# Performance work log

Hardware: AMD Instinct MI355X
Metric: run time of the kernel (lower is better)

Reference implementation:

```python
import jax, jax.numpy as jnp
import numpy as np

D_MODEL = 4096
NUM_HEADS = 64
DEPTH = D_MODEL // NUM_HEADS  # 64
B = 64   # must equal NUM_HEADS (quirk of original rope-after-split-heads code)
S = 64   # must equal NUM_HEADS (S*DEPTH must equal D_MODEL)


def setup_inputs() -> dict:
    key = jax.random.key(0)
    ks = jax.random.split(key, 9)
    scale = 1.0 / np.sqrt(D_MODEL)
    d = {"x": jax.random.normal(ks[0], (B, S, D_MODEL), dtype=jnp.float32)}
    for i, n in enumerate(["q", "k", "v", "o"]):
        d[f"w_{n}"] = jax.random.normal(ks[1 + i], (D_MODEL, D_MODEL), dtype=jnp.float32) * scale
        d[f"b_{n}"] = jax.random.normal(ks[5 + i], (D_MODEL,), dtype=jnp.float32) * 0.01
    return d


def _rope(x):
    # Faithful to the original: rope is applied to (B, H, S, depth) and treats
    # dim 1 (heads) as the 'sequence' axis, with inv_freq sized for full d_model.
    inv_freq = 1.0 / (10000.0 ** (jnp.arange(0, D_MODEL, 2, dtype=jnp.float32) / D_MODEL))
    pos = jnp.arange(x.shape[1], dtype=jnp.float32)[:, None]       # (H, 1)
    sinusoid = pos * inv_freq                                       # (H, d_model/2)
    sin = jnp.sin(sinusoid)[None, :, None, :]                       # (1, H, 1, d_model/2)
    cos = jnp.cos(sinusoid)[None, :, None, :]
    xr = x.reshape(x.shape[0], x.shape[1], -1, 2)                   # (B, H, S*depth/2, 2)
    real, imag = xr[..., 0], xr[..., 1]                             # (B, H, M) with M == d_model/2
    rot_real = real * cos - imag * sin                              # broadcasts to (1, B, H, M)
    rot_imag = real * sin + imag * cos
    return jnp.stack((rot_real, rot_imag), axis=-1).reshape(x.shape)


def reference(x, w_q, b_q, w_k, b_k, w_v, b_v, w_o, b_o):
    def split_heads(t):  # (B, S, d_model) -> (B, H, S, depth)
        return t.reshape(B, S, NUM_HEADS, DEPTH).transpose(0, 2, 1, 3)

    q = split_heads(x @ w_q.T + b_q)
    k = split_heads(x @ w_k.T + b_k)
    v = split_heads(x @ w_v.T + b_v)
    q = _rope(q)
    k = _rope(k)

    scores = jnp.einsum("bhqd,bhkd->bhqk", q, k) / np.sqrt(DEPTH).astype(np.float32)
    weights = jax.nn.softmax(scores, axis=-1)
    out = jnp.einsum("bhqk,bhkd->bhqd", weights, v)
    out = out.transpose(0, 2, 1, 3).reshape(B, S, D_MODEL)
    return out @ w_o.T + b_o
```

## Files before the change

kernel.cpp:

```cpp
#include <hip/hip_runtime.h>
#include <cstdint>
#include <cstddef>


typedef _Float16 half8 __attribute__((ext_vector_type(8)));
typedef float floatx4 __attribute__((ext_vector_type(4)));

#define NELT_W 16777216u
#define NEG_LOG2_10000_OVER_2048 (-0.0064881408103278559f)

__device__ __forceinline__ void gl_lds16(const void* g, void* l) {
    __builtin_amdgcn_global_load_lds(
        (const __attribute__((address_space(1))) void*)(void*)g,
        (__attribute__((address_space(3))) void*)l,
        16, 0, 0);
}

__global__ __launch_bounds__(256) void cast5_kernel(
    const float* __restrict__ x,  const float* __restrict__ wq,
    const float* __restrict__ wk, const float* __restrict__ wv,
    const float* __restrict__ wo,
    _Float16* __restrict__ xh, _Float16* __restrict__ wcat,
    _Float16* __restrict__ woh)
{
    const float* s;
    _Float16* d;
    switch (blockIdx.y) {
        case 0:  s = x;  d = xh;                 break;
        case 1:  s = wq; d = wcat;               break;
        case 2:  s = wk; d = wcat + NELT_W;      break;
        case 3:  s = wv; d = wcat + 2 * NELT_W;  break;
        default: s = wo; d = woh;                break;
    }
    int i0 = (blockIdx.x * 256 + threadIdx.x) * 8;
    int stride = gridDim.x * 256 * 8;
    for (int i = i0; i < (int)NELT_W; i += stride) {
        const float4 a = *(const float4*)(s + i);
        const float4 b = *(const float4*)(s + i + 4);
        half8 h;
        h[0] = (_Float16)a.x; h[1] = (_Float16)a.y;
        h[2] = (_Float16)a.z; h[3] = (_Float16)a.w;
        h[4] = (_Float16)b.x; h[5] = (_Float16)b.y;
        h[6] = (_Float16)b.z; h[7] = (_Float16)b.w;
        *(half8*)(d + i) = h;
    }
}

__global__ __launch_bounds__(256) void biascat_kernel(
    const float* __restrict__ bq, const float* __restrict__ bk,
    const float* __restrict__ bv, float* __restrict__ out)
{
    int i = blockIdx.x * 256 + threadIdx.x;
    if (i < 4096) {
        out[i]        = bq[i];
        out[4096 + i] = bk[i];
        out[8192 + i] = bv[i];
    }
}


#define STAGE(gb_, lb_, kt_, half_) do {                                      \
    const int R0_ = (half_) << 7;                                             \
    gl_lds16((gb_) + (size_t)R0_ * K + (kt_), (lb_) + R0_ * 64);              \
    gl_lds16((gb_) + (size_t)(R0_ + 64) * K + (kt_), (lb_) + (R0_ + 64) * 64);\
} while (0)

#define LDA2(bo_, ha_, m0_) do {                                              \
    const _Float16* pa_ = As + (bo_) + (size_t)(((ha_) << 7) + wg2 + fr) * 64;\
    _Pragma("unroll") for (int mt_ = (m0_); mt_ < (m0_) + 2; ++mt_) {         \
        af[mt_][0] = *(const half8*)(pa_ + mt_ * 1024 + sw0);                 \
        af[mt_][1] = *(const half8*)(pa_ + mt_ * 1024 + sw1);                 \
    }                                                                         \
} while (0)

#define LDB4(bo_, hb_, dst_) do {                                             \
    const _Float16* pb_ = Bs + (bo_) + (size_t)(((hb_) << 7) + wn2 + fr) * 64;\
    _Pragma("unroll") for (int nt_ = 0; nt_ < 2; ++nt_) {                     \
        dst_[nt_][0] = *(const half8*)(pb_ + nt_ * 1024 + sw0);               \
        dst_[nt_][1] = *(const half8*)(pb_ + nt_ * 1024 + sw1);               \
    }                                                                         \
} while (0)

#define MFMAQ(qm_, qn_, bq_) do {                                             \
    _Pragma("unroll") for (int s_ = 0; s_ < 2; ++s_)                          \
    _Pragma("unroll") for (int mt_ = 0; mt_ < 4; ++mt_)                       \
    _Pragma("unroll") for (int nt_ = 0; nt_ < 2; ++nt_)                       \
        acc[(qm_) * 4 + mt_][(qn_) * 2 + nt_] =                               \
            __builtin_amdgcn_mfma_f32_16x16x32_f16(                           \
                af[mt_][s_], bq_[nt_][s_],                                    \
                acc[(qm_) * 4 + mt_][(qn_) * 2 + nt_], 0, 0, 0);              \
} while (0)

#define TILE() do {                                                           \
    const int kt1_ = (t + 1) << 6;                                            \
    const int kt2_ = (t + 2) << 6;                                            \
    const bool s1_ = (t + 1 < NT);                                            \
    const bool s2_ = (t + 2 < NT);                                            \
                       \
    LDB4(bufo, 1, bq1);                                                       \
    if (s1_) STAGE(Ab, AsT + nbufo, kt1_, 1);                                 \
    __builtin_amdgcn_s_barrier();                                             \
    __builtin_amdgcn_s_setprio(1);                                            \
    MFMAQ(0, 0, bq0);                                                         \
    __builtin_amdgcn_s_setprio(0);                                            \
    __builtin_amdgcn_s_barrier();                                             \
             \
    if (s2_) STAGE(Ab, AsT + bufo, kt2_, 0);                                  \
    __builtin_amdgcn_s_barrier();                                             \
    __builtin_amdgcn_s_setprio(1);                                            \
    MFMAQ(0, 1, bq1);                                                         \
    __builtin_amdgcn_s_setprio(0);                                            \
    LDA2(bufo, 1, 0);                        \
    __builtin_amdgcn_s_barrier();                                             \
       \
    LDA2(bufo, 1, 2);                                                         \
    if (s2_) STAGE(Bb, BsT + bufo, kt2_, 0);                                  \
    __builtin_amdgcn_s_barrier();                                             \
    __builtin_amdgcn_s_setprio(1);                                            \
    MFMAQ(1, 0, bq0);                                                         \
    __builtin_amdgcn_s_setprio(0);                                            \
    __builtin_amdgcn_s_barrier();                                             \
        \
    if (s2_) STAGE(Bb, BsT + bufo, kt2_, 1);                                  \
    if (t < NT - 2) asm volatile("s_waitcnt vmcnt(6)" ::: "memory");          \
    else            asm volatile("s_waitcnt vmcnt(0)" ::: "memory");          \
    __builtin_amdgcn_s_barrier();                                             \
    __builtin_amdgcn_sched_barrier(0);   \
    if (s1_) LDB4(nbufo, 0, bq0);         \
    __builtin_amdgcn_s_setprio(1);                                            \
    MFMAQ(1, 1, bq1);                                                         \
    __builtin_amdgcn_s_setprio(0);                                            \
    if (s1_) { LDA2(nbufo, 0, 0); LDA2(nbufo, 0, 2); }          \
    __builtin_amdgcn_s_barrier();                                             \
} while (0)

template <int OUT_F16>
__global__ __launch_bounds__(512, 2) void gemm_nt_256(
    const _Float16* __restrict__ A, const _Float16* __restrict__ B,
    const float* __restrict__ bias, void* __restrict__ Cout,
    int M, int N, int K)
{
    __shared__ __align__(16) _Float16 As[2 * 256 * 64];
    __shared__ __align__(16) _Float16 Bs[2 * 256 * 64];

    const int tid = threadIdx.x;
    const int nwg  = gridDim.x;
    const int swz  = (blockIdx.x & 7) * (nwg >> 3) + (blockIdx.x >> 3);
    const int gn   = N >> 8;
    const int row0 = (swz / gn) << 8;
    const int col0 = (swz % gn) << 8;

    const int wave = tid >> 6;
    const int lane = tid & 63;
    const int wg2 = (wave >> 2) << 6;
    const int wn2 = (wave & 3) << 5;

    const int fr  = lane & 15;
    const int g4  = lane >> 4;
    const int sw0 = ((g4 ^ (fr & 7)) << 3);
    const int sw1 = (((4 + g4) ^ (fr & 7)) << 3);

    const int srow = tid >> 3;
    const int scol = ((tid & 7) ^ (srow & 7)) << 3;
    const _Float16* Ab = A + (size_t)(row0 + srow) * K + scol;
    const _Float16* Bb = B + (size_t)(col0 + srow) * K + scol;
    _Float16* AsT = As + tid * 8;
    _Float16* BsT = Bs + tid * 8;

    floatx4 acc[8][4];
#pragma unroll
    for (int i = 0; i < 8; i++)
#pragma unroll
        for (int j = 0; j < 4; j++) acc[i][j] = (floatx4){0.f, 0.f, 0.f, 0.f};

    half8 af[4][2], bq0[2][2], bq1[2][2];

    const int NT = K >> 6;

    STAGE(Ab, AsT, 0, 0);
    STAGE(Ab, AsT, 0, 1);
    STAGE(Bb, BsT, 0, 0);
    STAGE(Bb, BsT, 0, 1);
    STAGE(Ab, AsT + 16384, 64, 0);
    STAGE(Bb, BsT + 16384, 64, 0);
    STAGE(Bb, BsT + 16384, 64, 1);
    asm volatile("s_waitcnt vmcnt(6)" ::: "memory");
    __builtin_amdgcn_s_barrier();
    __builtin_amdgcn_sched_barrier(0);
    LDB4(0, 0, bq0);
    LDA2(0, 0, 0);
    LDA2(0, 0, 2);

    for (int tt = 0; tt < NT; tt += 2) {
        { const int t = tt;     const int bufo = 0;     const int nbufo = 16384; TILE(); }
        { const int t = tt + 1; const int bufo = 16384; const int nbufo = 0;     TILE(); }
    }

    const int crow = row0 + wg2 + (g4 << 2);
    const int ccol = col0 + wn2 + fr;
#pragma unroll
    for (int mi = 0; mi < 8; mi++) {
#pragma unroll
        for (int ni = 0; ni < 4; ni++) {
            const int gc = ccol + ((ni >> 1) << 7) + ((ni & 1) << 4);
            const float bv = bias[gc];
#pragma unroll
            for (int r2 = 0; r2 < 4; r2++) {
                const int gr = crow + ((mi >> 2) << 7) + ((mi & 3) << 4) + r2;
                const float v = acc[mi][ni][r2] + bv;
                if (OUT_F16)
                    ((_Float16*)Cout)[(size_t)gr * N + gc] = (_Float16)v;
                else
                    ((float*)Cout)[(size_t)gr * N + gc] = v;
            }
        }
    }
    (void)M;
}

__global__ __launch_bounds__(256) void attn_kernel(
    const _Float16* __restrict__ qkv, _Float16* __restrict__ out)
{
    __shared__ __align__(16) _Float16 qs[64][72];
    __shared__ __align__(16) _Float16 ks[64][72];
    __shared__ __align__(16) _Float16 vt[64][72];
    __shared__ __align__(16) _Float16 ps[4][16][72];

    const int tid  = threadIdx.x;
    const int bb   = blockIdx.x >> 6;
    const int hh   = blockIdx.x & 63;
    const int wave = tid >> 6;
    const int lane = tid & 63;
    const int r  = tid >> 2;
    const int cb = (tid & 3) * 8;
    const float fb = (float)bb;

    const _Float16* grow = qkv + (size_t)(bb * 64 + r) * 12288 + hh * 64;

#pragma unroll
    for (int u = 0; u < 2; u++) {
        const int c8 = cb + u * 32;
        half8 q8 = *(const half8*)(grow + c8);
        half8 k8 = *(const half8*)(grow + 4096 + c8);
        half8 v8 = *(const half8*)(grow + 8192 + c8);
#pragma unroll
        for (int p = 0; p < 4; p++) {
            const int m = r * 32 + (c8 >> 1) + p;
            const float theta = fb * exp2f((float)m * NEG_LOG2_10000_OVER_2048);
            float sn, cs;
            __sincosf(theta, &sn, &cs);
            const float qe = (float)q8[2 * p], qo = (float)q8[2 * p + 1];
            q8[2 * p]     = (_Float16)(qe * cs - qo * sn);
            q8[2 * p + 1] = (_Float16)(qe * sn + qo * cs);
            const float ke = (float)k8[2 * p], ko = (float)k8[2 * p + 1];
            k8[2 * p]     = (_Float16)(ke * cs - ko * sn);
            k8[2 * p + 1] = (_Float16)(ke * sn + ko * cs);
        }
        *(half8*)&qs[r][c8] = q8;
        *(half8*)&ks[r][c8] = k8;
#pragma unroll
        for (int j = 0; j < 8; j++) vt[c8 + j][r] = v8[j];
    }
    __syncthreads();

    const int fr = lane & 15;
    const int fc = (lane >> 4) * 8;

    floatx4 sa[4];
#pragma unroll
    for (int t = 0; t < 4; t++) sa[t] = (floatx4){0.f, 0.f, 0.f, 0.f};
    half8 a0 = *(const half8*)&qs[wave * 16 + fr][fc];
    half8 a1 = *(const half8*)&qs[wave * 16 + fr][fc + 32];
#pragma unroll
    for (int t = 0; t < 4; t++) {
        half8 kb0 = *(const half8*)&ks[t * 16 + fr][fc];
        half8 kb1 = *(const half8*)&ks[t * 16 + fr][fc + 32];
        sa[t] = __builtin_amdgcn_mfma_f32_16x16x32_f16(a0, kb0, sa[t], 0, 0, 0);
        sa[t] = __builtin_amdgcn_mfma_f32_16x16x32_f16(a1, kb1, sa[t], 0, 0, 0);
    }

#pragma unroll
    for (int i = 0; i < 4; i++) {
        float mx = -1e30f;
#pragma unroll
        for (int t = 0; t < 4; t++) mx = fmaxf(mx, sa[t][i]);
#pragma unroll
        for (int d = 1; d < 16; d <<= 1) mx = fmaxf(mx, __shfl_xor(mx, d));
        float sum = 0.f;
        float pv[4];
#pragma unroll
        for (int t = 0; t < 4; t++) {
            const float e = __expf((sa[t][i] - mx) * 0.125f);
            pv[t] = e;
            sum += e;
        }
#pragma unroll
        for (int d = 1; d < 16; d <<= 1) sum += __shfl_xor(sum, d);
        const float inv = 1.0f / sum;
        const int prow = ((lane >> 4) << 2) + i;
#pragma unroll
        for (int t = 0; t < 4; t++)
            ps[wave][prow][t * 16 + fr] = (_Float16)(pv[t] * inv);
    }

    half8 pa0 = *(const half8*)&ps[wave][fr][fc];
    half8 pa1 = *(const half8*)&ps[wave][fr][fc + 32];
    floatx4 oa[4];
#pragma unroll
    for (int t = 0; t < 4; t++) oa[t] = (floatx4){0.f, 0.f, 0.f, 0.f};
#pragma unroll
    for (int t = 0; t < 4; t++) {
        half8 vb0 = *(const half8*)&vt[t * 16 + fr][fc];
        half8 vb1 = *(const half8*)&vt[t * 16 + fr][fc + 32];
        oa[t] = __builtin_amdgcn_mfma_f32_16x16x32_f16(pa0, vb0, oa[t], 0, 0, 0);
        oa[t] = __builtin_amdgcn_mfma_f32_16x16x32_f16(pa1, vb1, oa[t], 0, 0, 0);
    }

    _Float16* obase = out + (size_t)(bb * 64) * 4096 + hh * 64;
#pragma unroll
    for (int t = 0; t < 4; t++)
#pragma unroll
        for (int i = 0; i < 4; i++) {
            const int sq = wave * 16 + ((lane >> 4) << 2) + i;
            obase[(size_t)sq * 4096 + t * 16 + fr] = (_Float16)oa[t][i];
        }
}

extern "C" void kernel_launch(void* const* d_in, const int* in_sizes, int n_in,
                              void* d_out, int out_size, void* d_ws, size_t ws_size,
                              hipStream_t stream)
{
    const float* x  = (const float*)d_in[0];
    const float* wq = (const float*)d_in[1];
    const float* bq = (const float*)d_in[2];
    const float* wk = (const float*)d_in[3];
    const float* bk = (const float*)d_in[4];
    const float* wv = (const float*)d_in[5];
    const float* bv = (const float*)d_in[6];
    const float* wo = (const float*)d_in[7];
    const float* bo = (const float*)d_in[8];

    char* ws = (char*)d_ws;
    _Float16* xh      = (_Float16*)(ws);
    _Float16* wcat    = (_Float16*)(ws + 33554432);
    _Float16* woh     = (_Float16*)(ws + 134217728);
    _Float16* qkv     = (_Float16*)(ws + 167772160);
    _Float16* attnbuf = (_Float16*)(ws + 268435456);
    float*    biascat = (float*)(ws + 301989888);

    cast5_kernel<<<dim3(1024, 5), dim3(256), 0, stream>>>(
        x, wq, wk, wv, wo, xh, wcat, woh);
    biascat_kernel<<<dim3(16), dim3(256), 0, stream>>>(bq, bk, bv, biascat);

    gemm_nt_256<1><<<dim3(768), dim3(512), 0, stream>>>(
        xh, wcat, biascat, qkv, 4096, 12288, 4096);

    attn_kernel<<<dim3(4096), dim3(256), 0, stream>>>(qkv, attnbuf);

    gemm_nt_256<0><<<dim3(256), dim3(512), 0, stream>>>(
        attnbuf, woh, bo, d_out, 4096, 4096, 4096);
}
```

Measured before the change: 878.3 us.

## Switch GEMM inner loop to 32x32x16 MFMA with restructured LDS fragment loads

```diff
diff --git a/kernel.cpp b/kernel.cpp
--- a/kernel.cpp
+++ b/kernel.cpp
@@ -5,6 +5,7 @@
 
 typedef _Float16 half8 __attribute__((ext_vector_type(8)));
 typedef float floatx4 __attribute__((ext_vector_type(4)));
+typedef float floatx16 __attribute__((ext_vector_type(16)));
 
 #define NELT_W 16777216u
 #define NEG_LOG2_10000_OVER_2048 (-0.0064881408103278559f)
@@ -59,36 +60,37 @@
 }
 
 
+#define BAR()   __builtin_amdgcn_s_barrier()
+#define SB0()   __builtin_amdgcn_sched_barrier(0)
+#define SETP1() __builtin_amdgcn_s_setprio(1)
+#define SETP0() __builtin_amdgcn_s_setprio(0)
+
 #define STAGE(gb_, lb_, kt_, half_) do {                                      \
     const int R0_ = (half_) << 7;                                             \
     gl_lds16((gb_) + (size_t)R0_ * K + (kt_), (lb_) + R0_ * 64);              \
     gl_lds16((gb_) + (size_t)(R0_ + 64) * K + (kt_), (lb_) + (R0_ + 64) * 64);\
 } while (0)
 
-#define LDA2(bo_, ha_, m0_) do {                                              \
-    const _Float16* pa_ = As + (bo_) + (size_t)(((ha_) << 7) + wg2 + fr) * 64;\
-    _Pragma("unroll") for (int mt_ = (m0_); mt_ < (m0_) + 2; ++mt_) {         \
-        af[mt_][0] = *(const half8*)(pa_ + mt_ * 1024 + sw0);                 \
-        af[mt_][1] = *(const half8*)(pa_ + mt_ * 1024 + sw1);                 \
-    }                                                                         \
-} while (0)
-
-#define LDB4(bo_, hb_, dst_) do {                                             \
-    const _Float16* pb_ = Bs + (bo_) + (size_t)(((hb_) << 7) + wn2 + fr) * 64;\
-    _Pragma("unroll") for (int nt_ = 0; nt_ < 2; ++nt_) {                     \
-        dst_[nt_][0] = *(const half8*)(pb_ + nt_ * 1024 + sw0);               \
-        dst_[nt_][1] = *(const half8*)(pb_ + nt_ * 1024 + sw1);               \
-    }                                                                         \
-} while (0)
-
-#define MFMAQ(qm_, qn_, bq_) do {                                             \
-    _Pragma("unroll") for (int s_ = 0; s_ < 2; ++s_)                          \
-    _Pragma("unroll") for (int mt_ = 0; mt_ < 4; ++mt_)                       \
-    _Pragma("unroll") for (int nt_ = 0; nt_ < 2; ++nt_)                       \
-        acc[(qm_) * 4 + mt_][(qn_) * 2 + nt_] =                               \
-            __builtin_amdgcn_mfma_f32_16x16x32_f16(                           \
-                af[mt_][s_], bq_[nt_][s_],                                    \
-                acc[(qm_) * 4 + mt_][(qn_) * 2 + nt_], 0, 0, 0);              \
+#define LDA32(bo_, ha_) do {                                                  \
+    const _Float16* pa_ = As + (bo_) +                                        \
+        (size_t)((((ha_) << 7) + wg2 + l31) * 64);                            \
+    _Pragma("unroll") for (int ks_ = 0; ks_ < 4; ++ks_)                       \
+    _Pragma("unroll") for (int mf_ = 0; mf_ < 2; ++mf_)                       \
+        af[mf_][ks_] = *(const half8*)(pa_ + mf_ * 2048 + swzk[ks_]);         \
+} while (0)
+
+#define LDB32(bo_, hb_, dst_) do {                                            \
+    const _Float16* pb_ = Bs + (bo_) +                                        \
+        (size_t)((((hb_) << 7) + wn2 + l31) * 64);                            \
+    _Pragma("unroll") for (int ks_ = 0; ks_ < 4; ++ks_)                       \
+        dst_[ks_] = *(const half8*)(pb_ + swzk[ks_]);                         \
+} while (0)
+
+#define MFMA8(mq_, nq_, bqv_) do {                                            \
+    _Pragma("unroll") for (int ks_ = 0; ks_ < 4; ++ks_)                       \
+    _Pragma("unroll") for (int mf_ = 0; mf_ < 2; ++mf_)                       \
+        acc[(mq_) * 2 + mf_][nq_] = __builtin_amdgcn_mfma_f32_32x32x16_f16(   \
+            af[mf_][ks_], bqv_[ks_], acc[(mq_) * 2 + mf_][nq_], 0, 0, 0);     \
 } while (0)
 
 #define TILE() do {                                                           \
@@ -96,42 +98,28 @@
     const int kt2_ = (t + 2) << 6;                                            \
     const bool s1_ = (t + 1 < NT);                                            \
     const bool s2_ = (t + 2 < NT);                                            \
-                       \
-    LDB4(bufo, 1, bq1);                                                       \
+       \
+    LDA32(bufo, 0);                                                           \
+    LDB32(bufo, 0, bq0);                                                      \
+    SETP1(); MFMA8(0, 0, bq0); SETP0();                                       \
+    LDB32(bufo, 1, bq1);                                                      \
     if (s1_) STAGE(Ab, AsT + nbufo, kt1_, 1);                                 \
-    __builtin_amdgcn_s_barrier();                                             \
-    __builtin_amdgcn_s_setprio(1);                                            \
-    MFMAQ(0, 0, bq0);                                                         \
-    __builtin_amdgcn_s_setprio(0);                                            \
-    __builtin_amdgcn_s_barrier();                                             \
-             \
+    SB0(); BAR();                                                             \
+                \
+    SETP1(); MFMA8(0, 1, bq1); SETP0();                                       \
+    LDA32(bufo, 1);                                                           \
     if (s2_) STAGE(Ab, AsT + bufo, kt2_, 0);                                  \
-    __builtin_amdgcn_s_barrier();                                             \
-    __builtin_amdgcn_s_setprio(1);                                            \
-    MFMAQ(0, 1, bq1);                                                         \
-    __builtin_amdgcn_s_setprio(0);                                            \
-    LDA2(bufo, 1, 0);                        \
-    __builtin_amdgcn_s_barrier();                                             \
-       \
-    LDA2(bufo, 1, 2);                                                         \
+    SB0(); BAR();                                                             \
+                                       \
+    SETP1(); MFMA8(1, 0, bq0); SETP0();                                       \
     if (s2_) STAGE(Bb, BsT + bufo, kt2_, 0);                                  \
-    __builtin_amdgcn_s_barrier();                                             \
-    __builtin_amdgcn_s_setprio(1);                                            \
-    MFMAQ(1, 0, bq0);                                                         \
-    __builtin_amdgcn_s_setprio(0);                                            \
-    __builtin_amdgcn_s_barrier();                                             \
-        \
+    SB0(); BAR();                                                             \
+         \
+    SETP1(); MFMA8(1, 1, bq1); SETP0();                                       \
     if (s2_) STAGE(Bb, BsT + bufo, kt2_, 1);                                  \
     if (t < NT - 2) asm volatile("s_waitcnt vmcnt(6)" ::: "memory");          \
     else            asm volatile("s_waitcnt vmcnt(0)" ::: "memory");          \
-    __builtin_amdgcn_s_barrier();                                             \
-    __builtin_amdgcn_sched_barrier(0);   \
-    if (s1_) LDB4(nbufo, 0, bq0);         \
-    __builtin_amdgcn_s_setprio(1);                                            \
-    MFMAQ(1, 1, bq1);                                                         \
-    __builtin_amdgcn_s_setprio(0);                                            \
-    if (s1_) { LDA2(nbufo, 0, 0); LDA2(nbufo, 0, 2); }          \
-    __builtin_amdgcn_s_barrier();                                             \
+    SB0(); BAR();                                                             \
 } while (0)
 
 template <int OUT_F16>
@@ -154,11 +142,13 @@
     const int lane = tid & 63;
     const int wg2 = (wave >> 2) << 6;
     const int wn2 = (wave & 3) << 5;
-
-    const int fr  = lane & 15;
-    const int g4  = lane >> 4;
-    const int sw0 = ((g4 ^ (fr & 7)) << 3);
-    const int sw1 = (((4 + g4) ^ (fr & 7)) << 3);
+    const int l31 = lane & 31;
+    const int hi  = lane >> 5;
+
+    int swzk[4];
+#pragma unroll
+    for (int ks = 0; ks < 4; ++ks)
+        swzk[ks] = (((ks * 2 + hi) ^ (lane & 7)) << 3);
 
     const int srow = tid >> 3;
     const int scol = ((tid & 7) ^ (srow & 7)) << 3;
@@ -167,13 +157,15 @@
     _Float16* AsT = As + tid * 8;
     _Float16* BsT = Bs + tid * 8;
 
-    floatx4 acc[8][4];
-#pragma unroll
-    for (int i = 0; i < 8; i++)
-#pragma unroll
-        for (int j = 0; j < 4; j++) acc[i][j] = (floatx4){0.f, 0.f, 0.f, 0.f};
-
-    half8 af[4][2], bq0[2][2], bq1[2][2];
+    floatx16 acc[4][2];
+#pragma unroll
+    for (int i = 0; i < 4; i++)
+#pragma unroll
+        for (int j = 0; j < 2; j++)
+#pragma unroll
+            for (int e = 0; e < 16; e++) acc[i][j][e] = 0.f;
+
+    half8 af[2][4], bq0[4], bq1[4];
 
     const int NT = K >> 6;
 
@@ -185,29 +177,27 @@
     STAGE(Bb, BsT + 16384, 64, 0);
     STAGE(Bb, BsT + 16384, 64, 1);
     asm volatile("s_waitcnt vmcnt(6)" ::: "memory");
-    __builtin_amdgcn_s_barrier();
-    __builtin_amdgcn_sched_barrier(0);
-    LDB4(0, 0, bq0);
-    LDA2(0, 0, 0);
-    LDA2(0, 0, 2);
+    SB0();
+    BAR();
 
     for (int tt = 0; tt < NT; tt += 2) {
         { const int t = tt;     const int bufo = 0;     const int nbufo = 16384; TILE(); }
         { const int t = tt + 1; const int bufo = 16384; const int nbufo = 0;     TILE(); }
     }
 
-    const int crow = row0 + wg2 + (g4 << 2);
-    const int ccol = col0 + wn2 + fr;
-#pragma unroll
-    for (int mi = 0; mi < 8; mi++) {
-#pragma unroll
-        for (int ni = 0; ni < 4; ni++) {
-            const int gc = ccol + ((ni >> 1) << 7) + ((ni & 1) << 4);
+    const int crow = row0 + wg2 + (hi << 2);
+    const int ccol = col0 + wn2 + l31;
+#pragma unroll
+    for (int mq = 0; mq < 4; ++mq) {
+        const int rbase = crow + ((mq >> 1) << 7) + ((mq & 1) << 5);
+#pragma unroll
+        for (int nf = 0; nf < 2; ++nf) {
+            const int gc = ccol + (nf << 7);
             const float bv = bias[gc];
 #pragma unroll
-            for (int r2 = 0; r2 < 4; r2++) {
-                const int gr = crow + ((mi >> 2) << 7) + ((mi & 3) << 4) + r2;
-                const float v = acc[mi][ni][r2] + bv;
+            for (int reg = 0; reg < 16; ++reg) {
+                const int gr = rbase + (reg & 3) + ((reg >> 2) << 3);
+                const float v = acc[mq][nf][reg] + bv;
                 if (OUT_F16)
                     ((_Float16*)Cout)[(size_t)gr * N + gc] = (_Float16)v;
                 else
```

New measurement: 925.6 us. 5.4% more time.

## Replace fine-grained interleaved GEMM pipeline with simple double-buffered tile loop

Applied to the files above, without the earlier changes.

```diff
diff --git a/kernel.cpp b/kernel.cpp
--- a/kernel.cpp
+++ b/kernel.cpp
@@ -59,79 +59,51 @@
 }
 
 
+#define BAR()   __builtin_amdgcn_s_barrier()
+#define SETP1() __builtin_amdgcn_s_setprio(1)
+#define SETP0() __builtin_amdgcn_s_setprio(0)
+
 #define STAGE(gb_, lb_, kt_, half_) do {                                      \
     const int R0_ = (half_) << 7;                                             \
     gl_lds16((gb_) + (size_t)R0_ * K + (kt_), (lb_) + R0_ * 64);              \
     gl_lds16((gb_) + (size_t)(R0_ + 64) * K + (kt_), (lb_) + (R0_ + 64) * 64);\
 } while (0)
 
-#define LDA2(bo_, ha_, m0_) do {                                              \
-    const _Float16* pa_ = As + (bo_) + (size_t)(((ha_) << 7) + wg2 + fr) * 64;\
-    _Pragma("unroll") for (int mt_ = (m0_); mt_ < (m0_) + 2; ++mt_) {         \
-        af[mt_][0] = *(const half8*)(pa_ + mt_ * 1024 + sw0);                 \
-        af[mt_][1] = *(const half8*)(pa_ + mt_ * 1024 + sw1);                 \
-    }                                                                         \
-} while (0)
-
-#define LDB4(bo_, hb_, dst_) do {                                             \
-    const _Float16* pb_ = Bs + (bo_) + (size_t)(((hb_) << 7) + wn2 + fr) * 64;\
-    _Pragma("unroll") for (int nt_ = 0; nt_ < 2; ++nt_) {                     \
-        dst_[nt_][0] = *(const half8*)(pb_ + nt_ * 1024 + sw0);               \
-        dst_[nt_][1] = *(const half8*)(pb_ + nt_ * 1024 + sw1);               \
-    }                                                                         \
-} while (0)
-
-#define MFMAQ(qm_, qn_, bq_) do {                                             \
-    _Pragma("unroll") for (int s_ = 0; s_ < 2; ++s_)                          \
-    _Pragma("unroll") for (int mt_ = 0; mt_ < 4; ++mt_)                       \
-    _Pragma("unroll") for (int nt_ = 0; nt_ < 2; ++nt_)                       \
-        acc[(qm_) * 4 + mt_][(qn_) * 2 + nt_] =                               \
-            __builtin_amdgcn_mfma_f32_16x16x32_f16(                           \
-                af[mt_][s_], bq_[nt_][s_],                                    \
-                acc[(qm_) * 4 + mt_][(qn_) * 2 + nt_], 0, 0, 0);              \
+#define LDAS(bo_, sw_) do {                                                   \
+    _Pragma("unroll") for (int mf_ = 0; mf_ < 8; ++mf_)                       \
+        af[mf_] = *(const half8*)(As + (bo_) +                                \
+            (size_t)((((mf_ >> 2) << 7) + wg2 + ((mf_ & 3) << 4) + fr) * 64)  \
+            + (sw_));                                                         \
+} while (0)
+
+#define LDBS(bo_, sw_) do {                                                   \
+    _Pragma("unroll") for (int nf_ = 0; nf_ < 4; ++nf_)                       \
+        bf[nf_] = *(const half8*)(Bs + (bo_) +                                \
+            (size_t)((((nf_ >> 1) << 7) + wn2 + ((nf_ & 1) << 4) + fr) * 64)  \
+            + (sw_));                                                         \
+} while (0)
+
+#define MFMAS() do {                                                          \
+    _Pragma("unroll") for (int nf_ = 0; nf_ < 4; ++nf_)                       \
+    _Pragma("unroll") for (int mf_ = 0; mf_ < 8; ++mf_)                       \
+        acc[mf_][nf_] = __builtin_amdgcn_mfma_f32_16x16x32_f16(               \
+            af[mf_], bf[nf_], acc[mf_][nf_], 0, 0, 0);                        \
 } while (0)
 
 #define TILE() do {                                                           \
     const int kt1_ = (t + 1) << 6;                                            \
-    const int kt2_ = (t + 2) << 6;                                            \
-    const bool s1_ = (t + 1 < NT);                                            \
-    const bool s2_ = (t + 2 < NT);                                            \
-                       \
-    LDB4(bufo, 1, bq1);                                                       \
-    if (s1_) STAGE(Ab, AsT + nbufo, kt1_, 1);                                 \
-    __builtin_amdgcn_s_barrier();                                             \
-    __builtin_amdgcn_s_setprio(1);                                            \
-    MFMAQ(0, 0, bq0);                                                         \
-    __builtin_amdgcn_s_setprio(0);                                            \
-    __builtin_amdgcn_s_barrier();                                             \
-             \
-    if (s2_) STAGE(Ab, AsT + bufo, kt2_, 0);                                  \
-    __builtin_amdgcn_s_barrier();                                             \
-    __builtin_amdgcn_s_setprio(1);                                            \
-    MFMAQ(0, 1, bq1);                                                         \
-    __builtin_amdgcn_s_setprio(0);                                            \
-    LDA2(bufo, 1, 0);                        \
-    __builtin_amdgcn_s_barrier();                                             \
-       \
-    LDA2(bufo, 1, 2);                                                         \
-    if (s2_) STAGE(Bb, BsT + bufo, kt2_, 0);                                  \
-    __builtin_amdgcn_s_barrier();                                             \
-    __builtin_amdgcn_s_setprio(1);                                            \
-    MFMAQ(1, 0, bq0);                                                         \
-    __builtin_amdgcn_s_setprio(0);                                            \
-    __builtin_amdgcn_s_barrier();                                             \
-        \
-    if (s2_) STAGE(Bb, BsT + bufo, kt2_, 1);                                  \
-    if (t < NT - 2) asm volatile("s_waitcnt vmcnt(6)" ::: "memory");          \
-    else            asm volatile("s_waitcnt vmcnt(0)" ::: "memory");          \
-    __builtin_amdgcn_s_barrier();                                             \
-    __builtin_amdgcn_sched_barrier(0);   \
-    if (s1_) LDB4(nbufo, 0, bq0);         \
-    __builtin_amdgcn_s_setprio(1);                                            \
-    MFMAQ(1, 1, bq1);                                                         \
-    __builtin_amdgcn_s_setprio(0);                                            \
-    if (s1_) { LDA2(nbufo, 0, 0); LDA2(nbufo, 0, 2); }          \
-    __builtin_amdgcn_s_barrier();                                             \
+    if (t + 1 < NT) {                                                         \
+        STAGE(Ab, AsT + nbufo, kt1_, 0);                                      \
+        STAGE(Ab, AsT + nbufo, kt1_, 1);                                      \
+        STAGE(Bb, BsT + nbufo, kt1_, 0);                                      \
+        STAGE(Bb, BsT + nbufo, kt1_, 1);                                      \
+    }                                                                         \
+    LDAS(bufo, sw0); LDBS(bufo, sw0);                                         \
+    SETP1(); MFMAS(); SETP0();                                                \
+    LDAS(bufo, sw1); LDBS(bufo, sw1);                                         \
+    SETP1(); MFMAS(); SETP0();                                                \
+    asm volatile("s_waitcnt vmcnt(0)" ::: "memory");                          \
+    BAR();                                                                    \
 } while (0)
 
 template <int OUT_F16>
@@ -173,7 +145,7 @@
 #pragma unroll
         for (int j = 0; j < 4; j++) acc[i][j] = (floatx4){0.f, 0.f, 0.f, 0.f};
 
-    half8 af[4][2], bq0[2][2], bq1[2][2];
+    half8 af[8], bf[4];
 
     const int NT = K >> 6;
 
@@ -181,15 +153,8 @@
     STAGE(Ab, AsT, 0, 1);
     STAGE(Bb, BsT, 0, 0);
     STAGE(Bb, BsT, 0, 1);
-    STAGE(Ab, AsT + 16384, 64, 0);
-    STAGE(Bb, BsT + 16384, 64, 0);
-    STAGE(Bb, BsT + 16384, 64, 1);
-    asm volatile("s_waitcnt vmcnt(6)" ::: "memory");
-    __builtin_amdgcn_s_barrier();
-    __builtin_amdgcn_sched_barrier(0);
-    LDB4(0, 0, bq0);
-    LDA2(0, 0, 0);
-    LDA2(0, 0, 2);
+    asm volatile("s_waitcnt vmcnt(0)" ::: "memory");
+    BAR();
 
     for (int tt = 0; tt < NT; tt += 2) {
         { const int t = tt;     const int bufo = 0;     const int nbufo = 16384; TILE(); }
```

Measured after the change: 1.583 ms. 80.2% more time.
